# Kernel optimization log

Hardware: AMD Instinct MI355X
Metric: run time of the kernel (lower is better)

The kernel has to match this reference:

```python
import jax, jax.numpy as jnp
import numpy as np

N_ATOMS = 8192
N_EDGES = 262144
N_MOL = 128
F = 128
R = 20
CUTOFF = 5.0
L = 3
EPS = 1e-8


def setup_inputs() -> dict:
    key = jax.random.key(0)
    ks = jax.random.split(key, 20)
    sc = 0.05  # weight init scale for numerical stability
    inp = {
        "z": jax.random.randint(ks[0], (N_ATOMS,), 0, 100, dtype=jnp.int32),
        "pos": jax.random.uniform(ks[1], (N_ATOMS, 3), dtype=jnp.float32),
        "edge_src": jax.random.randint(ks[2], (N_EDGES,), 0, N_ATOMS, dtype=jnp.int32),
        "edge_dst": jax.random.randint(ks[3], (N_EDGES,), 0, N_ATOMS, dtype=jnp.int32),
        "mol_idx": jnp.sort(jax.random.randint(ks[4], (N_ATOMS,), 0, N_MOL, dtype=jnp.int32)),
        "embed": jax.random.normal(ks[5], (100, F), dtype=jnp.float32) * sc,
        "msg_w1": jax.random.normal(ks[6], (L, F, F), dtype=jnp.float32) * sc,
        "msg_b1": jnp.zeros((L, F), jnp.float32),
        "msg_w2": jax.random.normal(ks[7], (L, F, 3 * F), dtype=jnp.float32) * sc,
        "msg_b2": jnp.zeros((L, 3 * F), jnp.float32),
        "rbf_w": jax.random.normal(ks[8], (L, R, 3 * F), dtype=jnp.float32) * sc,
        "rbf_b": jnp.zeros((L, 3 * F), jnp.float32),
        "upd_u": jax.random.normal(ks[9], (L, F, F), dtype=jnp.float32) * sc,
        "upd_v": jax.random.normal(ks[10], (L, F, F), dtype=jnp.float32) * sc,
        "upd_a1": jax.random.normal(ks[11], (L, 2 * F, F), dtype=jnp.float32) * sc,
        "upd_a1b": jnp.zeros((L, F), jnp.float32),
        "upd_a2": jax.random.normal(ks[12], (L, F, 3 * F), dtype=jnp.float32) * sc,
        "upd_a2b": jnp.zeros((L, 3 * F), jnp.float32),
        "out_w1": jax.random.normal(ks[13], (F, F), dtype=jnp.float32) * sc,
        "out_b1": jnp.zeros((F,), jnp.float32),
        "out_w2": jax.random.normal(ks[14], (F, 1), dtype=jnp.float32) * sc,
        "out_b2": jnp.zeros((1,), jnp.float32),
    }
    return inp


def _painn_forward(z, pos, edge_src, edge_dst, mol_idx, embed,
                   msg_w1, msg_b1, msg_w2, msg_b2, rbf_w, rbf_b,
                   upd_u, upd_v, upd_a1, upd_a1b, upd_a2, upd_a2b,
                   out_w1, out_b1, out_w2, out_b2):
    n = z.shape[0]
    s = embed[z]                                  # [N,F]
    v = jnp.zeros((n, 3, F), s.dtype)             # [N,3,F]

    rij = pos[edge_dst] - pos[edge_src]           # [E,3]
    d = jnp.sqrt(jnp.sum(rij * rij, axis=-1) + EPS)  # [E]
    unit = rij / d[:, None]                       # [E,3]
    freq = jnp.arange(1, R + 1, dtype=s.dtype) * (jnp.pi / CUTOFF)
    rbf = jnp.sin(d[:, None] * freq[None, :]) / d[:, None]          # [E,R]
    fc = 0.5 * (jnp.cos(jnp.pi * d / CUTOFF) + 1.0) * (d < CUTOFF)  # [E]

    for l in range(L):
        # --- message block ---
        phi = jax.nn.silu(s @ msg_w1[l] + msg_b1[l]) @ msg_w2[l] + msg_b2[l]  # [N,3F]
        wfilt = (rbf @ rbf_w[l] + rbf_b[l]) * fc[:, None]                      # [E,3F]
        m = phi[edge_src] * wfilt                                              # [E,3F]
        ds_e, dvv, dvs = m[:, :F], m[:, F:2 * F], m[:, 2 * F:]
        ds = jax.ops.segment_sum(ds_e, edge_dst, num_segments=n)
        dv_e = v[edge_src] * dvv[:, None, :] + unit[:, :, None] * dvs[:, None, :]  # [E,3,F]
        dv = jax.ops.segment_sum(dv_e, edge_dst, num_segments=n)
        s = s + ds
        v = v + dv
        # --- update block ---
        uv = jnp.einsum('ncf,fg->ncg', v, upd_u[l])   # [N,3,F]
        vv = jnp.einsum('ncf,fg->ncg', v, upd_v[l])   # [N,3,F]
        vv_norm = jnp.sqrt(jnp.sum(vv * vv, axis=1) + EPS)  # [N,F]
        a = jax.nn.silu(jnp.concatenate([s, vv_norm], axis=-1) @ upd_a1[l] + upd_a1b[l])
        a = a @ upd_a2[l] + upd_a2b[l]                # [N,3F]
        a_vv, a_sv, a_ss = a[:, :F], a[:, F:2 * F], a[:, 2 * F:]
        s = s + a_ss + a_sv * jnp.sum(uv * vv, axis=1)
        v = v + a_vv[:, None, :] * uv

    atom_out = jax.nn.silu(s @ out_w1 + out_b1) @ out_w2 + out_b2  # [N,1]
    return jax.ops.segment_sum(atom_out, mol_idx, num_segments=N_MOL)  # [M,1]


def reference(z, pos, edge_src, edge_dst, mol_idx, embed,
              msg_w1, msg_b1, msg_w2, msg_b2, rbf_w, rbf_b,
              upd_u, upd_v, upd_a1, upd_a1b, upd_a2, upd_a2b,
              out_w1, out_b1, out_w2, out_b2):
    return _painn_forward(z, pos, edge_src, edge_dst, mol_idx, embed,
                          msg_w1, msg_b1, msg_w2, msg_b2, rbf_w, rbf_b,
                          upd_u, upd_v, upd_a1, upd_a1b, upd_a2, upd_a2b,
                          out_w1, out_b1, out_w2, out_b2)
```

## Files before the change

kernel.cpp:

```cpp
#include <hip/hip_runtime.h>
#include <hip/hip_bf16.h>
#include <math.h>

#define N_ATOMS 8192
#define N_EDGES 262144
#define N_MOL   128
#define FDIM    128
#define RDIM    20
#define LLAYERS 3
#define CUTOFF  5.0f
#define EPSV    1e-8f
#define PI_F    3.14159265358979323846f

typedef __attribute__((ext_vector_type(8))) short bf16x8;
typedef __attribute__((ext_vector_type(4))) float f32x4;

#define VPLANE 1048576

__device__ __forceinline__ ushort f2bf(float x) {
    uint b = __float_as_uint(x);
    return (ushort)((b + 0x7fffu + ((b >> 16) & 1u)) >> 16);
}

__global__ void k_wconv(const float* __restrict__ w1, const float* __restrict__ w2,
                        const float* __restrict__ uu, const float* __restrict__ uvw,
                        const float* __restrict__ a1, const float* __restrict__ a2,
                        const float* __restrict__ ow1, ushort* __restrict__ WT) {
    int i = blockIdx.x * 256 + threadIdx.x;
    float v;
    if (i < 49152) {
        int idx = i; int l = idx >> 14; idx &= 16383;
        int n = idx >> 7, k = idx & 127;
        v = w1[l*16384 + k*128 + n];
    } else if (i < 196608) {
        int idx = i - 49152; int l = idx / 49152; idx -= l * 49152;
        int n = idx >> 7, k = idx & 127;
        v = w2[l*49152 + k*384 + n];
    } else if (i < 294912) {
        int idx = i - 196608; int l = idx >> 15; idx &= 32767;
        int n = idx >> 7, k = idx & 127;
        v = (n < 128) ? uu[l*16384 + k*128 + n] : uvw[l*16384 + k*128 + (n-128)];
    } else if (i < 393216) {
        int idx = i - 294912; int l = idx >> 15; idx &= 32767;
        int n = idx >> 8, k = idx & 255;
        v = a1[l*32768 + k*128 + n];
    } else if (i < 540672) {
        int idx = i - 393216; int l = idx / 49152; idx -= l * 49152;
        int n = idx >> 7, k = idx & 127;
        v = a2[l*49152 + k*384 + n];
    } else {
        int idx = i - 540672;
        int n = idx >> 7, k = idx & 127;
        v = ow1[k*128 + n];
    }
    WT[i] = f2bf(v);
}

__global__ void k_embed(const int* __restrict__ z, const float* __restrict__ embed,
                        float* __restrict__ S, ushort* __restrict__ SBF) {
    int i = blockIdx.x * 256 + threadIdx.x;
    int a = i >> 7, k = i & 127;
    float v = embed[(size_t)z[a] * FDIM + k];
    S[i] = v; SBF[i] = f2bf(v);
}

__global__ void k_hist(const int* __restrict__ edst, int* __restrict__ CNT) {
    int e = blockIdx.x * 256 + threadIdx.x;
    if (e < N_EDGES) atomicAdd(&CNT[edst[e]], 1);
}

__global__ __launch_bounds__(1024) void k_scan(const int* __restrict__ CNT,
                                               int* __restrict__ OFF, int* __restrict__ CUR) {
    __shared__ int part[1024];
    int t = threadIdx.x;
    int loc[8];
    int run = 0;
    #pragma unroll
    for (int i = 0; i < 8; i++) { int c = CNT[t*8 + i]; loc[i] = run; run += c; }
    part[t] = run;
    __syncthreads();
    for (int off = 1; off < 1024; off <<= 1) {
        int v = 0;
        if (t >= off) v = part[t - off];
        __syncthreads();
        part[t] += v;
        __syncthreads();
    }
    int ebase = (t > 0) ? part[t-1] : 0;
    #pragma unroll
    for (int i = 0; i < 8; i++) { int o = ebase + loc[i]; OFF[t*8+i] = o; CUR[t*8+i] = o; }
    if (t == 1023) OFF[8192] = part[1023];
}

__global__ void k_pos(const int* __restrict__ edst, int* __restrict__ CUR,
                      int* __restrict__ POS) {
    int e = blockIdx.x * 256 + threadIdx.x;
    if (e < N_EDGES) POS[e] = atomicAdd(&CUR[edst[e]], 1);
}

__global__ void k_edges(const float* __restrict__ pos, const int* __restrict__ esrc,
                        const int* __restrict__ edst, const int* __restrict__ POS,
                        float* __restrict__ RBF, float* __restrict__ UNITFC,
                        int* __restrict__ SRCS) {
    int e = blockIdx.x * 256 + threadIdx.x;
    if (e >= N_EDGES) return;
    int s = esrc[e], d = edst[e];
    int p = POS[e];
    float rx = pos[d*3+0] - pos[s*3+0];
    float ry = pos[d*3+1] - pos[s*3+1];
    float rz = pos[d*3+2] - pos[s*3+2];
    float dd = sqrtf(rx*rx + ry*ry + rz*rz + EPSV);
    float inv = 1.0f / dd;
    float fc = (dd < CUTOFF) ? 0.5f * (cosf(dd * (PI_F / CUTOFF)) + 1.0f) : 0.0f;
    float4 u4; u4.x = rx*inv; u4.y = ry*inv; u4.z = rz*inv; u4.w = fc;
    *(float4*)&UNITFC[(size_t)p*4] = u4;
    SRCS[p] = s;
    float rb[RDIM];
    #pragma unroll
    for (int r = 0; r < RDIM; r++) {
        float freq = (float)(r + 1) * (PI_F / CUTOFF);
        rb[r] = sinf(dd * freq) * inv;
    }
    float4* out = (float4*)&RBF[(size_t)p * RDIM];
    #pragma unroll
    for (int q = 0; q < 5; q++) {
        float4 o; o.x = rb[q*4]; o.y = rb[q*4+1]; o.z = rb[q*4+2]; o.w = rb[q*4+3];
        out[q] = o;
    }
}

__global__ __launch_bounds__(256) void k_msg(
    const ushort* __restrict__ SBF, const ushort* __restrict__ W1T, const float* __restrict__ b1,
    const ushort* __restrict__ W2T, const float* __restrict__ b2, ushort* __restrict__ PHIB)
{
    int tid = threadIdx.x;
    int w = tid >> 6, l = tid & 63;
    int bm = blockIdx.x * 16;
    int lrow = l & 15, lk = (l >> 4) * 8;
    __shared__ ushort Hs[16][136];

    f32x4 acc[2] = {{0.f,0.f,0.f,0.f},{0.f,0.f,0.f,0.f}};
    #pragma unroll
    for (int k0 = 0; k0 < 128; k0 += 32) {
        bf16x8 af = *(const bf16x8*)&SBF[(size_t)(bm + lrow)*128 + k0 + lk];
        #pragma unroll
        for (int t = 0; t < 2; t++) {
            int n = (2*w + t)*16 + lrow;
            bf16x8 bf = *(const bf16x8*)&W1T[(size_t)n*128 + k0 + lk];
            acc[t] = __builtin_amdgcn_mfma_f32_16x16x32_bf16(af, bf, acc[t], 0, 0, 0);
        }
    }
    #pragma unroll
    for (int t = 0; t < 2; t++) {
        int col = (2*w + t)*16 + lrow;
        float bv = b1[col];
        #pragma unroll
        for (int j = 0; j < 4; j++) {
            int row = (l >> 4)*4 + j;
            float val = acc[t][j] + bv;
            val = val / (1.0f + __expf(-val));
            Hs[row][col] = f2bf(val);
        }
    }
    __syncthreads();

    f32x4 acc2[6];
    #pragma unroll
    for (int t = 0; t < 6; t++) acc2[t] = (f32x4){0.f,0.f,0.f,0.f};
    #pragma unroll
    for (int k0 = 0; k0 < 128; k0 += 32) {
        bf16x8 af = *(const bf16x8*)&Hs[lrow][k0 + lk];
        #pragma unroll
        for (int t = 0; t < 6; t++) {
            int n = (6*w + t)*16 + lrow;
            bf16x8 bf = *(const bf16x8*)&W2T[(size_t)n*128 + k0 + lk];
            acc2[t] = __builtin_amdgcn_mfma_f32_16x16x32_bf16(af, bf, acc2[t], 0, 0, 0);
        }
    }
    #pragma unroll
    for (int t = 0; t < 6; t++) {
        int col = (6*w + t)*16 + lrow;
        float bv = b2[col];
        #pragma unroll
        for (int j = 0; j < 4; j++) {
            int row = bm + (l >> 4)*4 + j;
            PHIB[(size_t)row*384 + col] = f2bf(acc2[t][j] + bv);
        }
    }
}

__global__ __launch_bounds__(192) void k_aggregate(
    const ushort* __restrict__ PHIB, const ushort* __restrict__ VBFA,
    float* __restrict__ S, ushort* __restrict__ SBF,
    float* __restrict__ V, ushort* __restrict__ VBFB,
    const float* __restrict__ RBF, const float* __restrict__ UNITFC,
    const int* __restrict__ SRCS, const int* __restrict__ OFF,
    const float* __restrict__ rbfw, const float* __restrict__ rbfb)
{
    int a = blockIdx.x;
    int tid = threadIdx.x;
    int g = tid >> 6;
    int c0 = 2 * (tid & 63);

    float2 w[RDIM];
    const float* wc = rbfw + g*128 + c0;
    #pragma unroll
    for (int r = 0; r < RDIM; r++) { w[r].x = wc[r*384]; w[r].y = wc[r*384 + 1]; }
    float2 bb; bb.x = rbfb[g*128 + c0]; bb.y = rbfb[g*128 + c0 + 1];

    __shared__ int sSrc[64];
    __shared__ float4 sRBF[320];
    __shared__ float4 sUFC[64];
    __shared__ float avs[3][128];

    int beg = OFF[a], end = OFF[a + 1];
    float2 d; d.x = 0.f; d.y = 0.f;
    float2 A0, A1, A2v;
    A0.x=A0.y=A1.x=A1.y=A2v.x=A2v.y=0.f;

    for (int p0 = beg; p0 < end; p0 += 64) {
        int n = end - p0; if (n > 64) n = 64;
        __syncthreads();
        if (tid < n) sSrc[tid] = SRCS[p0 + tid];
        for (int i = tid; i < n; i += 192)
            sUFC[i] = *(const float4*)(UNITFC + (size_t)(p0 + i) * 4);
        {
            const float4* rsrc = (const float4*)(RBF + (size_t)p0 * RDIM);
            for (int i = tid; i < n*5; i += 192) sRBF[i] = rsrc[i];
        }
        __syncthreads();

        uint phA[4], u0A[4], u1A[4], u2A[4];
        uint phB[4], u0B[4], u1B[4], u2B[4];

        auto grpLoad = [&](int base, uint* ph, uint* u0, uint* u1, uint* u2) {
            #pragma unroll
            for (int j = 0; j < 4; j++) {
                int q = base + j;
                int src = sSrc[(q < n) ? q : 0];
                size_t pb = (size_t)src * 128;
                ph[j] = *(const uint*)&PHIB[(size_t)src*384 + g*128 + c0];
                if (g == 1) {
                    u0[j] = *(const uint*)&VBFA[pb + c0];
                    u1[j] = *(const uint*)&VBFA[pb + VPLANE + c0];
                    u2[j] = *(const uint*)&VBFA[pb + 2*VPLANE + c0];
                }
            }
        };
        grpLoad(0, phA, u0A, u1A, u2A);
        for (int q0 = 0; q0 < n; q0 += 4) {
            if (q0 + 4 < n) grpLoad(q0 + 4, phB, u0B, u1B, u2B);
            #pragma unroll
            for (int j = 0; j < 4; j++) {
                int q = q0 + j;
                if (q >= n) break;
                float4 r0 = sRBF[q*5+0], r1 = sRBF[q*5+1], r2 = sRBF[q*5+2],
                       r3 = sRBF[q*5+3], r4 = sRBF[q*5+4];
                float4 ufc = sUFC[q];
                float2 f = bb;
                f.x += r0.x*w[0].x;   f.y += r0.x*w[0].y;
                f.x += r0.y*w[1].x;   f.y += r0.y*w[1].y;
                f.x += r0.z*w[2].x;   f.y += r0.z*w[2].y;
                f.x += r0.w*w[3].x;   f.y += r0.w*w[3].y;
                f.x += r1.x*w[4].x;   f.y += r1.x*w[4].y;
                f.x += r1.y*w[5].x;   f.y += r1.y*w[5].y;
                f.x += r1.z*w[6].x;   f.y += r1.z*w[6].y;
                f.x += r1.w*w[7].x;   f.y += r1.w*w[7].y;
                f.x += r2.x*w[8].x;   f.y += r2.x*w[8].y;
                f.x += r2.y*w[9].x;   f.y += r2.y*w[9].y;
                f.x += r2.z*w[10].x;  f.y += r2.z*w[10].y;
                f.x += r2.w*w[11].x;  f.y += r2.w*w[11].y;
                f.x += r3.x*w[12].x;  f.y += r3.x*w[12].y;
                f.x += r3.y*w[13].x;  f.y += r3.y*w[13].y;
                f.x += r3.z*w[14].x;  f.y += r3.z*w[14].y;
                f.x += r3.w*w[15].x;  f.y += r3.w*w[15].y;
                f.x += r4.x*w[16].x;  f.y += r4.x*w[16].y;
                f.x += r4.y*w[17].x;  f.y += r4.y*w[17].y;
                f.x += r4.z*w[18].x;  f.y += r4.z*w[18].y;
                f.x += r4.w*w[19].x;  f.y += r4.w*w[19].y;
                uint up = phA[j];
                float m0 = __uint_as_float(up << 16)         * (f.x * ufc.w);
                float m1 = __uint_as_float(up & 0xffff0000u) * (f.y * ufc.w);
                if (g == 0) {
                    d.x += m0; d.y += m1;
                } else if (g == 1) {
                    A0.x  += __uint_as_float(u0A[j] << 16)         * m0;
                    A0.y  += __uint_as_float(u0A[j] & 0xffff0000u) * m1;
                    A1.x  += __uint_as_float(u1A[j] << 16)         * m0;
                    A1.y  += __uint_as_float(u1A[j] & 0xffff0000u) * m1;
                    A2v.x += __uint_as_float(u2A[j] << 16)         * m0;
                    A2v.y += __uint_as_float(u2A[j] & 0xffff0000u) * m1;
                } else {
                    A0.x  += ufc.x * m0; A0.y  += ufc.x * m1;
                    A1.x  += ufc.y * m0; A1.y  += ufc.y * m1;
                    A2v.x += ufc.z * m0; A2v.y += ufc.z * m1;
                }
            }
            #pragma unroll
            for (int j = 0; j < 4; j++) {
                phA[j] = phB[j]; u0A[j] = u0B[j]; u1A[j] = u1B[j]; u2A[j] = u2B[j];
            }
        }
    }

    if (g == 1) {
        avs[0][c0] = A0.x;  avs[0][c0+1] = A0.y;
        avs[1][c0] = A1.x;  avs[1][c0+1] = A1.y;
        avs[2][c0] = A2v.x; avs[2][c0+1] = A2v.y;
    }
    __syncthreads();
    if (g == 0) {
        size_t sb = (size_t)a*128 + c0;
        float2 s2 = *(float2*)&S[sb];
        s2.x += d.x; s2.y += d.y;
        *(float2*)&S[sb] = s2;
        SBF[sb] = f2bf(s2.x); SBF[sb+1] = f2bf(s2.y);
    } else if (g == 2) {
        float own0[3] = {A0.x, A1.x, A2v.x};
        float own1[3] = {A0.y, A1.y, A2v.y};
        #pragma unroll
        for (int c = 0; c < 3; c++) {
            size_t vb = (size_t)c*VPLANE + (size_t)a*128 + c0;
            float2 vi = *(const float2*)&V[vb];
            vi.x += avs[c][c0]     + own0[c];
            vi.y += avs[c][c0 + 1] + own1[c];
            *(float2*)&V[vb] = vi;
            VBFB[vb] = f2bf(vi.x); VBFB[vb+1] = f2bf(vi.y);
        }
    }
}

__global__ __launch_bounds__(256) void k_upd(
    const ushort* __restrict__ VBFB, const ushort* __restrict__ UVT,
    const ushort* __restrict__ SBF_in,
    const ushort* __restrict__ A1T, const float* __restrict__ a1b,
    const ushort* __restrict__ A2T, const float* __restrict__ a2b,
    float* __restrict__ S, ushort* __restrict__ SBF,
    float* __restrict__ V, ushort* __restrict__ VBFA)
{
    int tid = threadIdx.x;
    int w = tid >> 6, l = tid & 63;
    int bm = blockIdx.x * 16;
    int lrow = l & 15, lk = (l >> 4) * 8;
    __shared__ ushort sVVN[16][136];
    __shared__ ushort Hs[16][136];

    f32x4 au[3][2], av[3][2];
    #pragma unroll
    for (int c = 0; c < 3; c++)
        #pragma unroll
        for (int t = 0; t < 2; t++) {
            au[c][t] = (f32x4){0.f,0.f,0.f,0.f};
            av[c][t] = (f32x4){0.f,0.f,0.f,0.f};
        }
    #pragma unroll
    for (int k0 = 0; k0 < 128; k0 += 32) {
        bf16x8 af[3];
        #pragma unroll
        for (int c = 0; c < 3; c++)
            af[c] = *(const bf16x8*)&VBFB[(size_t)c*VPLANE + (size_t)(bm + lrow)*128 + k0 + lk];
        #pragma unroll
        for (int t = 0; t < 2; t++) {
            int nu = (2*w + t)*16 + lrow;
            bf16x8 bu = *(const bf16x8*)&UVT[(size_t)nu*128 + k0 + lk];
            bf16x8 bv = *(const bf16x8*)&UVT[(size_t)(nu + 128)*128 + k0 + lk];
            #pragma unroll
            for (int c = 0; c < 3; c++) {
                au[c][t] = __builtin_amdgcn_mfma_f32_16x16x32_bf16(af[c], bu, au[c][t], 0, 0, 0);
                av[c][t] = __builtin_amdgcn_mfma_f32_16x16x32_bf16(af[c], bv, av[c][t], 0, 0, 0);
            }
        }
    }
    float dotr[2][4], uvr[3][2][4];
    #pragma unroll
    for (int t = 0; t < 2; t++) {
        int k = (2*w + t)*16 + lrow;
        #pragma unroll
        for (int j = 0; j < 4; j++) {
            int row = (l >> 4)*4 + j;
            float u0 = au[0][t][j], u1 = au[1][t][j], u2 = au[2][t][j];
            float v0 = av[0][t][j], v1 = av[1][t][j], v2 = av[2][t][j];
            uvr[0][t][j] = u0; uvr[1][t][j] = u1; uvr[2][t][j] = u2;
            dotr[t][j] = u0*v0 + u1*v1 + u2*v2;
            sVVN[row][k] = f2bf(sqrtf(v0*v0 + v1*v1 + v2*v2 + EPSV));
        }
    }
    __syncthreads();

    f32x4 acc[2] = {{0.f,0.f,0.f,0.f},{0.f,0.f,0.f,0.f}};
    #pragma unroll
    for (int k0 = 0; k0 < 256; k0 += 32) {
        bf16x8 af;
        if (k0 < 128) af = *(const bf16x8*)&SBF_in[(size_t)(bm + lrow)*128 + k0 + lk];
        else          af = *(const bf16x8*)&sVVN[lrow][k0 + lk - 128];
        #pragma unroll
        for (int t = 0; t < 2; t++) {
            int n = (2*w + t)*16 + lrow;
            bf16x8 bf = *(const bf16x8*)&A1T[(size_t)n*256 + k0 + lk];
            acc[t] = __builtin_amdgcn_mfma_f32_16x16x32_bf16(af, bf, acc[t], 0, 0, 0);
        }
    }
    #pragma unroll
    for (int t = 0; t < 2; t++) {
        int col = (2*w + t)*16 + lrow;
        float bv = a1b[col];
        #pragma unroll
        for (int j = 0; j < 4; j++) {
            int row = (l >> 4)*4 + j;
            float val = acc[t][j] + bv;
            val = val / (1.0f + __expf(-val));
            Hs[row][col] = f2bf(val);
        }
    }
    __syncthreads();

    f32x4 c_vv[2], c_sv[2], c_ss[2];
    #pragma unroll
    for (int t = 0; t < 2; t++) {
        c_vv[t] = (f32x4){0.f,0.f,0.f,0.f};
        c_sv[t] = (f32x4){0.f,0.f,0.f,0.f};
        c_ss[t] = (f32x4){0.f,0.f,0.f,0.f};
    }
    #pragma unroll
    for (int k0 = 0; k0 < 128; k0 += 32) {
        bf16x8 af = *(const bf16x8*)&Hs[lrow][k0 + lk];
        #pragma unroll
        for (int t = 0; t < 2; t++) {
            int n0 = (2*w + t)*16 + lrow;
            bf16x8 b0 = *(const bf16x8*)&A2T[(size_t)n0*128 + k0 + lk];
            bf16x8 b1 = *(const bf16x8*)&A2T[(size_t)(n0 + 128)*128 + k0 + lk];
            bf16x8 b2 = *(const bf16x8*)&A2T[(size_t)(n0 + 256)*128 + k0 + lk];
            c_vv[t] = __builtin_amdgcn_mfma_f32_16x16x32_bf16(af, b0, c_vv[t], 0, 0, 0);
            c_sv[t] = __builtin_amdgcn_mfma_f32_16x16x32_bf16(af, b1, c_sv[t], 0, 0, 0);
            c_ss[t] = __builtin_amdgcn_mfma_f32_16x16x32_bf16(af, b2, c_ss[t], 0, 0, 0);
        }
    }
    #pragma unroll
    for (int t = 0; t < 2; t++) {
        int k = (2*w + t)*16 + lrow;
        float b_vv = a2b[k], b_sv = a2b[128 + k], b_ss = a2b[256 + k];
        #pragma unroll
        for (int j = 0; j < 4; j++) {
            int a = bm + (l >> 4)*4 + j;
            size_t base = (size_t)a*128 + k;
            float vv = c_vv[t][j] + b_vv;
            float sv = c_sv[t][j] + b_sv;
            float ss = c_ss[t][j] + b_ss;
            float sn = S[base] + ss + sv * dotr[t][j];
            S[base] = sn; SBF[base] = f2bf(sn);
            #pragma unroll
            for (int c = 0; c < 3; c++) {
                size_t vb = (size_t)c*VPLANE + base;
                float nv = V[vb] + vv * uvr[c][t][j];
                V[vb] = nv; VBFA[vb] = f2bf(nv);
            }
        }
    }
}

__global__ __launch_bounds__(64) void k_readout(
    const ushort* __restrict__ SBF, const ushort* __restrict__ OW1T,
    const float* __restrict__ b1, const float* __restrict__ w2,
    const float* __restrict__ b2v, float* __restrict__ AOUT)
{
    int l = threadIdx.x;
    int bm = blockIdx.x * 16;
    int lrow = l & 15, lk = (l >> 4) * 8;
    __shared__ float Hs[16][132];

    f32x4 acc[8];
    #pragma unroll
    for (int t = 0; t < 8; t++) acc[t] = (f32x4){0.f,0.f,0.f,0.f};
    #pragma unroll
    for (int k0 = 0; k0 < 128; k0 += 32) {
        bf16x8 af = *(const bf16x8*)&SBF[(size_t)(bm + lrow)*128 + k0 + lk];
        #pragma unroll
        for (int t = 0; t < 8; t++) {
            bf16x8 bf = *(const bf16x8*)&OW1T[(size_t)(t*16 + lrow)*128 + k0 + lk];
            acc[t] = __builtin_amdgcn_mfma_f32_16x16x32_bf16(af, bf, acc[t], 0, 0, 0);
        }
    }
    #pragma unroll
    for (int t = 0; t < 8; t++) {
        int col = t*16 + lrow;
        float bv = b1[col];
        #pragma unroll
        for (int j = 0; j < 4; j++) {
            int row = (l >> 4)*4 + j;
            float val = acc[t][j] + bv;
            Hs[row][col] = val / (1.0f + __expf(-val));
        }
    }
    __syncthreads();
    if (l < 16) {
        float s = b2v[0];
        #pragma unroll 8
        for (int k = 0; k < 128; k++) s += Hs[l][k] * w2[k];
        AOUT[bm + l] = s;
    }
}

__global__ void k_molsum(const float* __restrict__ AOUT, const int* __restrict__ mol,
                         float* __restrict__ out) {
    __shared__ float acc[N_MOL];
    int t = threadIdx.x;
    if (t < N_MOL) acc[t] = 0.f;
    __syncthreads();
    for (int i = blockIdx.x * 256 + t; i < N_ATOMS; i += 256 * 32)
        atomicAdd(&acc[mol[i]], AOUT[i]);
    __syncthreads();
    if (t < N_MOL) atomicAdd(&out[t], acc[t]);
}

extern "C" void kernel_launch(void* const* d_in, const int* in_sizes, int n_in,
                              void* d_out, int out_size, void* d_ws, size_t ws_size,
                              hipStream_t stream) {
    const int*   z      = (const int*)d_in[0];
    const float* pos    = (const float*)d_in[1];
    const int*   esrc   = (const int*)d_in[2];
    const int*   edst   = (const int*)d_in[3];
    const int*   mol    = (const int*)d_in[4];
    const float* embed  = (const float*)d_in[5];
    const float* msg_w1 = (const float*)d_in[6];
    const float* msg_b1 = (const float*)d_in[7];
    const float* msg_w2 = (const float*)d_in[8];
    const float* msg_b2 = (const float*)d_in[9];
    const float* rbf_w  = (const float*)d_in[10];
    const float* rbf_b  = (const float*)d_in[11];
    const float* upd_u  = (const float*)d_in[12];
    const float* upd_v  = (const float*)d_in[13];
    const float* upd_a1 = (const float*)d_in[14];
    const float* upd_a1b= (const float*)d_in[15];
    const float* upd_a2 = (const float*)d_in[16];
    const float* upd_a2b= (const float*)d_in[17];
    const float* out_w1 = (const float*)d_in[18];
    const float* out_b1 = (const float*)d_in[19];
    const float* out_w2 = (const float*)d_in[20];
    const float* out_b2 = (const float*)d_in[21];

    float* ws = (float*)d_ws;
    float* S      = ws; ws += 1048576;
    float* V      = ws; ws += 3145728;
    float* RBF    = ws; ws += 5242880;
    float* UNITFC = ws; ws += 1048576;
    float* AOUT   = ws; ws += 8192;
    ushort* PHIB  = (ushort*)ws; ws += 1572864;
    ushort* VBFA  = (ushort*)ws; ws += 1572864;
    ushort* VBFB  = (ushort*)ws; ws += 1572864;
    ushort* SBF   = (ushort*)ws; ws += 524288;
    ushort* WT    = (ushort*)ws; ws += 278528;
    int* CNT  = (int*)ws;
    int* OFF  = CNT + 8192;
    int* CUR  = OFF + 8193;
    int* POS  = CUR + 8192;
    int* SRCS = POS + N_EDGES;

    hipMemsetAsync(V, 0, 3145728 * sizeof(float), stream);
    hipMemsetAsync(VBFA, 0, 3145728 * sizeof(ushort), stream);
    hipMemsetAsync(CNT, 0, 8192 * sizeof(int), stream);

    k_wconv<<<2176, 256, 0, stream>>>(msg_w1, msg_w2, upd_u, upd_v, upd_a1, upd_a2, out_w1, WT);
    k_embed<<<4096, 256, 0, stream>>>(z, embed, S, SBF);
    k_hist<<<1024, 256, 0, stream>>>(edst, CNT);
    k_scan<<<1, 1024, 0, stream>>>(CNT, OFF, CUR);
    k_pos<<<1024, 256, 0, stream>>>(edst, CUR, POS);
    k_edges<<<1024, 256, 0, stream>>>(pos, esrc, edst, POS, RBF, UNITFC, SRCS);

    for (int l = 0; l < LLAYERS; l++) {
        const ushort* W1T = WT + l*16384;
        const ushort* W2T = WT + 49152  + l*49152;
        const ushort* UVT = WT + 196608 + l*32768;
        const ushort* A1T = WT + 294912 + l*32768;
        const ushort* A2T = WT + 393216 + l*49152;

        k_msg<<<512, 256, 0, stream>>>(SBF, W1T, msg_b1 + (size_t)l*128,
                                       W2T, msg_b2 + (size_t)l*384, PHIB);
        k_aggregate<<<8192, 192, 0, stream>>>(PHIB, VBFA, S, SBF, V, VBFB, RBF, UNITFC,
            SRCS, OFF, rbf_w + (size_t)l*20*384, rbf_b + (size_t)l*384);
        k_upd<<<512, 256, 0, stream>>>(VBFB, UVT, SBF, A1T, upd_a1b + (size_t)l*128,
            A2T, upd_a2b + (size_t)l*384, S, SBF, V, VBFA);
    }

    k_readout<<<512, 64, 0, stream>>>(SBF, WT + 540672, out_b1, out_w2, out_b2, AOUT);
    hipMemsetAsync(d_out, 0, N_MOL * sizeof(float), stream);
    k_molsum<<<32, 256, 0, stream>>>(AOUT, mol, (float*)d_out);
}
```

Measured before the change: 619.2 us.

## Deepen aggregate gather prefetch and fuse edge-position and molecule-sum kernels

The aggregate loop now keeps three groups of four edges' gathered PHI/V values in flight in a rotating schedule instead of double-buffering one group, to hide more global gather latency. The separate k_pos kernel is folded into k_edges by doing the slot atomicAdd inline, and k_molsum is removed by having k_readout atomically add each atom's output straight into the molecule sum. These cut launches and the POS/AOUT round trips. The costs are more registers in the aggregate kernel, which may lower occupancy, more global atomics on out, and loads past n that rely on the clamped source index.

```diff
diff --git a/kernel.cpp b/kernel.cpp
--- a/kernel.cpp
+++ b/kernel.cpp
@@ -92,20 +92,14 @@
     if (t == 1023) OFF[8192] = part[1023];
 }
 
-__global__ void k_pos(const int* __restrict__ edst, int* __restrict__ CUR,
-                      int* __restrict__ POS) {
-    int e = blockIdx.x * 256 + threadIdx.x;
-    if (e < N_EDGES) POS[e] = atomicAdd(&CUR[edst[e]], 1);
-}
-
 __global__ void k_edges(const float* __restrict__ pos, const int* __restrict__ esrc,
-                        const int* __restrict__ edst, const int* __restrict__ POS,
+                        const int* __restrict__ edst, int* __restrict__ CUR,
                         float* __restrict__ RBF, float* __restrict__ UNITFC,
                         int* __restrict__ SRCS) {
     int e = blockIdx.x * 256 + threadIdx.x;
     if (e >= N_EDGES) return;
     int s = esrc[e], d = edst[e];
-    int p = POS[e];
+    int p = atomicAdd(&CUR[d], 1);
     float rx = pos[d*3+0] - pos[s*3+0];
     float ry = pos[d*3+1] - pos[s*3+1];
     float rz = pos[d*3+2] - pos[s*3+2];
@@ -232,6 +226,7 @@
 
         uint phA[4], u0A[4], u1A[4], u2A[4];
         uint phB[4], u0B[4], u1B[4], u2B[4];
+        uint phC[4], u0C[4], u1C[4], u2C[4];
 
         auto grpLoad = [&](int base, uint* ph, uint* u0, uint* u1, uint* u2) {
             #pragma unroll
@@ -247,12 +242,10 @@
                 }
             }
         };
-        grpLoad(0, phA, u0A, u1A, u2A);
-        for (int q0 = 0; q0 < n; q0 += 4) {
-            if (q0 + 4 < n) grpLoad(q0 + 4, phB, u0B, u1B, u2B);
+        auto grpComp = [&](int base, uint* ph, uint* u0, uint* u1, uint* u2) {
             #pragma unroll
             for (int j = 0; j < 4; j++) {
-                int q = q0 + j;
+                int q = base + j;
                 if (q >= n) break;
                 float4 r0 = sRBF[q*5+0], r1 = sRBF[q*5+1], r2 = sRBF[q*5+2],
                        r3 = sRBF[q*5+3], r4 = sRBF[q*5+4];
@@ -278,28 +271,36 @@
                 f.x += r4.y*w[17].x;  f.y += r4.y*w[17].y;
                 f.x += r4.z*w[18].x;  f.y += r4.z*w[18].y;
                 f.x += r4.w*w[19].x;  f.y += r4.w*w[19].y;
-                uint up = phA[j];
+                uint up = ph[j];
                 float m0 = __uint_as_float(up << 16)         * (f.x * ufc.w);
                 float m1 = __uint_as_float(up & 0xffff0000u) * (f.y * ufc.w);
                 if (g == 0) {
                     d.x += m0; d.y += m1;
                 } else if (g == 1) {
-                    A0.x  += __uint_as_float(u0A[j] << 16)         * m0;
-                    A0.y  += __uint_as_float(u0A[j] & 0xffff0000u) * m1;
-                    A1.x  += __uint_as_float(u1A[j] << 16)         * m0;
-                    A1.y  += __uint_as_float(u1A[j] & 0xffff0000u) * m1;
-                    A2v.x += __uint_as_float(u2A[j] << 16)         * m0;
-                    A2v.y += __uint_as_float(u2A[j] & 0xffff0000u) * m1;
+                    A0.x  += __uint_as_float(u0[j] << 16)         * m0;
+                    A0.y  += __uint_as_float(u0[j] & 0xffff0000u) * m1;
+                    A1.x  += __uint_as_float(u1[j] << 16)         * m0;
+                    A1.y  += __uint_as_float(u1[j] & 0xffff0000u) * m1;
+                    A2v.x += __uint_as_float(u2[j] << 16)         * m0;
+                    A2v.y += __uint_as_float(u2[j] & 0xffff0000u) * m1;
                 } else {
                     A0.x  += ufc.x * m0; A0.y  += ufc.x * m1;
                     A1.x  += ufc.y * m0; A1.y  += ufc.y * m1;
                     A2v.x += ufc.z * m0; A2v.y += ufc.z * m1;
                 }
             }
-            #pragma unroll
-            for (int j = 0; j < 4; j++) {
-                phA[j] = phB[j]; u0A[j] = u0B[j]; u1A[j] = u1B[j]; u2A[j] = u2B[j];
-            }
+        };
+
+        grpLoad(0, phA, u0A, u1A, u2A);
+        grpLoad(4, phB, u0B, u1B, u2B);
+        grpLoad(8, phC, u0C, u1C, u2C);
+        for (int q0 = 0; q0 < n; q0 += 12) {
+            grpComp(q0,      phA, u0A, u1A, u2A);
+            grpLoad(q0 + 12, phA, u0A, u1A, u2A);
+            grpComp(q0 + 4,  phB, u0B, u1B, u2B);
+            grpLoad(q0 + 16, phB, u0B, u1B, u2B);
+            grpComp(q0 + 8,  phC, u0C, u1C, u2C);
+            grpLoad(q0 + 20, phC, u0C, u1C, u2C);
         }
     }
 
@@ -461,7 +462,8 @@
 __global__ __launch_bounds__(64) void k_readout(
     const ushort* __restrict__ SBF, const ushort* __restrict__ OW1T,
     const float* __restrict__ b1, const float* __restrict__ w2,
-    const float* __restrict__ b2v, float* __restrict__ AOUT)
+    const float* __restrict__ b2v, const int* __restrict__ mol,
+    float* __restrict__ out)
 {
     int l = threadIdx.x;
     int bm = blockIdx.x * 16;
@@ -496,20 +498,8 @@
         float s = b2v[0];
         #pragma unroll 8
         for (int k = 0; k < 128; k++) s += Hs[l][k] * w2[k];
-        AOUT[bm + l] = s;
-    }
-}
-
-__global__ void k_molsum(const float* __restrict__ AOUT, const int* __restrict__ mol,
-                         float* __restrict__ out) {
-    __shared__ float acc[N_MOL];
-    int t = threadIdx.x;
-    if (t < N_MOL) acc[t] = 0.f;
-    __syncthreads();
-    for (int i = blockIdx.x * 256 + t; i < N_ATOMS; i += 256 * 32)
-        atomicAdd(&acc[mol[i]], AOUT[i]);
-    __syncthreads();
-    if (t < N_MOL) atomicAdd(&out[t], acc[t]);
+        atomicAdd(&out[mol[bm + l]], s);
+    }
 }
 
 extern "C" void kernel_launch(void* const* d_in, const int* in_sizes, int n_in,
@@ -543,7 +533,6 @@
     float* V      = ws; ws += 3145728;
     float* RBF    = ws; ws += 5242880;
     float* UNITFC = ws; ws += 1048576;
-    float* AOUT   = ws; ws += 8192;
     ushort* PHIB  = (ushort*)ws; ws += 1572864;
     ushort* VBFA  = (ushort*)ws; ws += 1572864;
     ushort* VBFB  = (ushort*)ws; ws += 1572864;
@@ -552,19 +541,18 @@
     int* CNT  = (int*)ws;
     int* OFF  = CNT + 8192;
     int* CUR  = OFF + 8193;
-    int* POS  = CUR + 8192;
-    int* SRCS = POS + N_EDGES;
+    int* SRCS = CUR + 8192;
 
     hipMemsetAsync(V, 0, 3145728 * sizeof(float), stream);
     hipMemsetAsync(VBFA, 0, 3145728 * sizeof(ushort), stream);
     hipMemsetAsync(CNT, 0, 8192 * sizeof(int), stream);
+    hipMemsetAsync(d_out, 0, N_MOL * sizeof(float), stream);
 
     k_wconv<<<2176, 256, 0, stream>>>(msg_w1, msg_w2, upd_u, upd_v, upd_a1, upd_a2, out_w1, WT);
     k_embed<<<4096, 256, 0, stream>>>(z, embed, S, SBF);
     k_hist<<<1024, 256, 0, stream>>>(edst, CNT);
     k_scan<<<1, 1024, 0, stream>>>(CNT, OFF, CUR);
-    k_pos<<<1024, 256, 0, stream>>>(edst, CUR, POS);
-    k_edges<<<1024, 256, 0, stream>>>(pos, esrc, edst, POS, RBF, UNITFC, SRCS);
+    k_edges<<<1024, 256, 0, stream>>>(pos, esrc, edst, CUR, RBF, UNITFC, SRCS);
 
     for (int l = 0; l < LLAYERS; l++) {
         const ushort* W1T = WT + l*16384;
@@ -581,7 +569,6 @@
             A2T, upd_a2b + (size_t)l*384, S, SBF, V, VBFA);
     }
 
-    k_readout<<<512, 64, 0, stream>>>(SBF, WT + 540672, out_b1, out_w2, out_b2, AOUT);
-    hipMemsetAsync(d_out, 0, N_MOL * sizeof(float), stream);
-    k_molsum<<<32, 256, 0, stream>>>(AOUT, mol, (float*)d_out);
-}
+    k_readout<<<512, 64, 0, stream>>>(SBF, WT + 540672, out_b1, out_w2, out_b2,
+                                      mol, (float*)d_out);
+}
```

After: 704.3 us. +13.7%, slower.
